# Performance work log

Measured on AMD Instinct MI355X. Metric: run time of the kernel, lower is better.

## Reference

```python
import jax, jax.numpy as jnp
import numpy as np

B, S, E, H = 2, 2048, 1024, 16
HD = E // H


def setup_inputs() -> dict:
    key = jax.random.key(0)
    ks = jax.random.split(key, 5)
    scale = 0.02
    return {
        "x": jax.random.normal(ks[0], (B, S, E), dtype=jnp.float32),
        "qkv_w": jax.random.normal(ks[1], (3 * E, E), dtype=jnp.float32) * scale,
        "qkv_b": jax.random.normal(ks[2], (3 * E,), dtype=jnp.float32) * scale,
        "out_w": jax.random.normal(ks[3], (E, E), dtype=jnp.float32) * scale,
        "out_b": jax.random.normal(ks[4], (E,), dtype=jnp.float32) * scale,
    }


def reference(x, qkv_w, qkv_b, out_w, out_b):
    b, s, e = x.shape
    scale = 1.0 / jnp.sqrt(jnp.float32(HD))
    # fused QKV projection: torch Linear is x @ W.T + b
    qkv = x @ qkv_w.T + qkv_b                       # [b, s, 3e]
    qkv = qkv.reshape(b, s, 3, H, HD)
    qkv = jnp.transpose(qkv, (2, 0, 3, 1, 4))       # [3, b, h, s, hd]
    q, k, v = qkv[0], qkv[1], qkv[2]
    scores = jnp.einsum('bhqd,bhkd->bhqk', q, k) * scale
    # causal mask (atmask=True): mask strictly upper triangle
    causal = jnp.triu(jnp.ones((s, s), dtype=bool), k=1)
    scores = jnp.where(causal, -jnp.inf, scores)
    attn = jax.nn.softmax(scores, axis=-1)          # dropout p=0.0 -> identity
    out = jnp.einsum('bhqk,bhkd->bhqd', attn, v)    # [b, h, s, hd]
    out = jnp.transpose(out, (0, 2, 1, 3)).reshape(b, s, e)
    return out @ out_w.T + out_b
```

## Files before the change

kernel.cpp:

```cpp
#include <hip/hip_runtime.h>
#include <cmath>

typedef __attribute__((ext_vector_type(8))) __bf16 bf16x8;
typedef __attribute__((ext_vector_type(8))) unsigned short ushort8v;
typedef __attribute__((ext_vector_type(4))) float f32x4;

__device__ inline unsigned short f2bf(float f) {
    unsigned int u = __float_as_uint(f);
    unsigned int r = (u + 0x7fffu + ((u >> 16) & 1u)) >> 16;
    return (unsigned short)r;
}

__device__ inline bf16x8 ld8(const unsigned short* p) {
    uint4 v = *(const uint4*)p;
    return __builtin_bit_cast(bf16x8, v);
}

__device__ inline f32x4 mfma16(bf16x8 a, bf16x8 b, f32x4 c) {
    return __builtin_amdgcn_mfma_f32_16x16x32_bf16(a, b, c, 0, 0, 0);
}

__device__ inline unsigned pk2t(float a, float b) {
    return __builtin_amdgcn_perm(__float_as_uint(b), __float_as_uint(a), 0x07060302u);
}

__device__ inline void gl_lds16(const unsigned short* g, const unsigned short* l) {
    __builtin_amdgcn_global_load_lds(
        (const __attribute__((address_space(1))) void*)(unsigned long long)g,
        (__attribute__((address_space(3))) void*)(unsigned)(unsigned long long)l,
        16, 0, 0);
}

#define NX4  1048576
#define NW14 786432
#define NW24 262144
__global__ __launch_bounds__(256) void cvt3(const float* __restrict__ x,
                                            const float* __restrict__ w1,
                                            const float* __restrict__ w2,
                                            unsigned short* __restrict__ xb,
                                            unsigned short* __restrict__ w1b,
                                            unsigned short* __restrict__ w2b) {
    int i = blockIdx.x * 256 + threadIdx.x;
    const float* src;
    unsigned short* dst;
    int off;
    if (i < NX4)              { src = x;  dst = xb;  off = i; }
    else if (i < NX4 + NW14)  { src = w1; dst = w1b; off = i - NX4; }
    else                      { src = w2; dst = w2b; off = i - NX4 - NW14; }
    float4 v = ((const float4*)src)[off];
    ushort4 o;
    o.x = f2bf(v.x); o.y = f2bf(v.y); o.z = f2bf(v.z); o.w = f2bf(v.w);
    ((ushort4*)dst)[off] = o;
}

__global__ __launch_bounds__(256) void gemm_out(const unsigned short* __restrict__ A,
                                                const unsigned short* __restrict__ B,
                                                const float* __restrict__ bias,
                                                float* __restrict__ C,
                                                int M, int N, int K) {
    __shared__ __align__(16) unsigned short As0[64 * 32];
    __shared__ __align__(16) unsigned short Bs0[128 * 32];
    __shared__ __align__(16) unsigned short As1[64 * 32];
    __shared__ __align__(16) unsigned short Bs1[128 * 32];
    const int m0 = blockIdx.y * 64;
    const int n0 = blockIdx.x * 128;
    const int t = threadIdx.x;
    const int wave = t >> 6, lane = t & 63;
    const int l16 = lane & 15, quad = lane >> 4;
    const int wm = (wave >> 1) * 32, wn = (wave & 1) * 64;

    f32x4 acc[2][4] = {};

    const int ra = t >> 2, ka = (t & 3) * 8;
    const int b1 = 256 + t;
    const int rb0 = t >> 2, kb0 = (t & 3) * 8;
    const int rb1 = b1 >> 2, kb1 = (b1 & 3) * 8;

    for (int k0 = 0; k0 < K; k0 += 64) {
        __syncthreads();
        gl_lds16(A + (size_t)(m0 + ra) * K + k0 + ka,        As0 + t * 8);
        gl_lds16(B + (size_t)(n0 + rb0) * K + k0 + kb0,      Bs0 + t * 8);
        gl_lds16(B + (size_t)(n0 + rb1) * K + k0 + kb1,      Bs0 + b1 * 8);
        gl_lds16(A + (size_t)(m0 + ra) * K + k0 + 32 + ka,   As1 + t * 8);
        gl_lds16(B + (size_t)(n0 + rb0) * K + k0 + 32 + kb0, Bs1 + t * 8);
        gl_lds16(B + (size_t)(n0 + rb1) * K + k0 + 32 + kb1, Bs1 + b1 * 8);
        __syncthreads();

        bf16x8 af[2], bfr[4];
        #pragma unroll
        for (int i = 0; i < 2; ++i)
            af[i] = ld8(As0 + (wm + i * 16 + l16) * 32 + quad * 8);
        #pragma unroll
        for (int j = 0; j < 4; ++j)
            bfr[j] = ld8(Bs0 + (wn + j * 16 + l16) * 32 + quad * 8);
        #pragma unroll
        for (int i = 0; i < 2; ++i)
            #pragma unroll
            for (int j = 0; j < 4; ++j)
                acc[i][j] = mfma16(af[i], bfr[j], acc[i][j]);

        #pragma unroll
        for (int i = 0; i < 2; ++i)
            af[i] = ld8(As1 + (wm + i * 16 + l16) * 32 + quad * 8);
        #pragma unroll
        for (int j = 0; j < 4; ++j)
            bfr[j] = ld8(Bs1 + (wn + j * 16 + l16) * 32 + quad * 8);
        #pragma unroll
        for (int i = 0; i < 2; ++i)
            #pragma unroll
            for (int j = 0; j < 4; ++j)
                acc[i][j] = mfma16(af[i], bfr[j], acc[i][j]);
    }

    #pragma unroll
    for (int i = 0; i < 2; ++i) {
        #pragma unroll
        for (int j = 0; j < 4; ++j) {
            int col = n0 + wn + j * 16 + l16;
            float bv = bias[col];
            #pragma unroll
            for (int r = 0; r < 4; ++r) {
                int row = m0 + wm + i * 16 + quad * 4 + r;
                C[(size_t)row * N + col] = acc[i][j][r] + bv;
            }
        }
    }
}

__global__ __launch_bounds__(256) void gemm_qkv(const unsigned short* __restrict__ A,
                                                const unsigned short* __restrict__ B,
                                                const float* __restrict__ bias,
                                                unsigned short* __restrict__ qp,
                                                unsigned short* __restrict__ kvp,
                                                int M, int N, int K) {
    __shared__ __align__(16) unsigned short Ep[16384];
    unsigned short* As0 = Ep;
    unsigned short* Bs0 = Ep + 4096;
    unsigned short* As1 = Ep + 8192;
    unsigned short* Bs1 = Ep + 12288;
    const int m0 = blockIdx.y * 128;
    const int n0 = blockIdx.x * 128;
    const int t = threadIdx.x;
    const int wave = t >> 6, lane = t & 63;
    const int l16 = lane & 15, quad = lane >> 4;
    const int wm = (wave >> 1) * 64, wn = (wave & 1) * 64;

    f32x4 acc[4][4] = {};

    const int ra = t >> 2, ka = (t & 3) * 8;

    for (int k0 = 0; k0 < K; k0 += 64) {
        __syncthreads();
        gl_lds16(A + (size_t)(m0 + ra) * K + k0 + ka,           As0 + t * 8);
        gl_lds16(A + (size_t)(m0 + 64 + ra) * K + k0 + ka,      As0 + 2048 + t * 8);
        gl_lds16(B + (size_t)(n0 + ra) * K + k0 + ka,           Bs0 + t * 8);
        gl_lds16(B + (size_t)(n0 + 64 + ra) * K + k0 + ka,      Bs0 + 2048 + t * 8);
        gl_lds16(A + (size_t)(m0 + ra) * K + k0 + 32 + ka,      As1 + t * 8);
        gl_lds16(A + (size_t)(m0 + 64 + ra) * K + k0 + 32 + ka, As1 + 2048 + t * 8);
        gl_lds16(B + (size_t)(n0 + ra) * K + k0 + 32 + ka,      Bs1 + t * 8);
        gl_lds16(B + (size_t)(n0 + 64 + ra) * K + k0 + 32 + ka, Bs1 + 2048 + t * 8);
        __syncthreads();

        bf16x8 af[4], bfr[4];
        #pragma unroll
        for (int i = 0; i < 4; ++i)
            af[i] = ld8(As0 + (wm + i * 16 + l16) * 32 + quad * 8);
        #pragma unroll
        for (int j = 0; j < 4; ++j)
            bfr[j] = ld8(Bs0 + (wn + j * 16 + l16) * 32 + quad * 8);
        #pragma unroll
        for (int i = 0; i < 4; ++i)
            #pragma unroll
            for (int j = 0; j < 4; ++j)
                acc[i][j] = mfma16(af[i], bfr[j], acc[i][j]);

        #pragma unroll
        for (int i = 0; i < 4; ++i)
            af[i] = ld8(As1 + (wm + i * 16 + l16) * 32 + quad * 8);
        #pragma unroll
        for (int j = 0; j < 4; ++j)
            bfr[j] = ld8(Bs1 + (wn + j * 16 + l16) * 32 + quad * 8);
        #pragma unroll
        for (int i = 0; i < 4; ++i)
            #pragma unroll
            for (int j = 0; j < 4; ++j)
                acc[i][j] = mfma16(af[i], bfr[j], acc[i][j]);
    }

    __syncthreads();
    const int b = m0 >> 11;

    if (n0 < 1024) {
        #pragma unroll
        for (int j = 0; j < 4; ++j) {
            int cl = wn + j * 16 + l16;
            float bv = bias[n0 + cl];
            int hrel = cl >> 6, d = cl & 63;
            int half = d >> 5, qd = d & 31;
            int obase = hrel * 8192 + half * 512 + (qd >> 3) * 128 + quad * 32 + (qd & 7);
            #pragma unroll
            for (int i = 0; i < 4; ++i) {
                int ob = obase + ((wm + i * 16) >> 4) * 1024;
                #pragma unroll
                for (int r = 0; r < 4; ++r)
                    Ep[ob + r * 8] = f2bf((acc[i][j][r] + bv) * 0.180336880f);
            }
        }
        __syncthreads();
        const int h0 = n0 >> 6, qt0 = (m0 & 2047) >> 4;
        #pragma unroll
        for (int k = 0; k < 8; ++k) {
            int u = t + 256 * k;
            int cq = u >> 7, within = u & 127;
            int bh = b * 16 + h0 + (cq >> 3);
            int qt = qt0 + (cq & 7);
            *(uint4*)(qp + (size_t)(bh * 128 + qt) * 1024 + within * 8) =
                *(const uint4*)(Ep + u * 8);
        }
    } else if (n0 < 2048) {
        const int f2 = (quad & 1) * 2, qh = 4 * (quad >> 1);
        #pragma unroll
        for (int j = 0; j < 4; ++j) {
            int cl = wn + j * 16 + l16;
            float bv = bias[n0 + cl];
            int hrel = cl >> 6, d = cl & 63;
            int fbit0 = d >> 5, qd = d & 31;
            int obase = hrel * 8192 + (f2 | fbit0) * 512 +
                        (qd >> 3) * 128 + qh * 8 + (qd & 7);
            #pragma unroll
            for (int i = 0; i < 4; ++i) {
                int ob = obase + ((wm >> 5) + (i >> 1)) * 2048 + (i & 1) * 64;
                #pragma unroll
                for (int r = 0; r < 4; ++r)
                    Ep[ob + r * 8] = f2bf(acc[i][j][r] + bv);
            }
        }
        __syncthreads();
        const int h0 = (n0 - 1024) >> 6, tile0 = (m0 & 2047) >> 5;
        #pragma unroll
        for (int k = 0; k < 8; ++k) {
            int u = t + 256 * k;
            int ck = u >> 8, within = u & 255;
            int bh = b * 16 + h0 + (ck >> 2);
            int tile = tile0 + (ck & 3);
            *(uint4*)(kvp + (size_t)(bh * 64 + tile) * 4096 + within * 8) =
                *(const uint4*)(Ep + u * 8);
        }
    } else {
        const int kr = quad >> 1, e4 = (quad & 1) * 4;
        #pragma unroll
        for (int j = 0; j < 4; ++j) {
            int cl = wn + j * 16 + l16;
            float bv = bias[n0 + cl];
            int hrel = cl >> 6, d = cl & 63;
            int tn = d >> 4, l16v = d & 15;
            int obase = hrel * 8192 + tn * 512 + (kr * 16 + l16v) * 8 + e4;
            #pragma unroll
            for (int i = 0; i < 4; ++i) {
                int ob = obase + ((wm >> 5) + (i >> 1)) * 2048 + (i & 1) * 256;
                unsigned short tmp[4];
                #pragma unroll
                for (int r = 0; r < 4; ++r) tmp[r] = f2bf(acc[i][j][r] + bv);
                *(unsigned long long*)(Ep + ob) = *(const unsigned long long*)tmp;
            }
        }
        __syncthreads();
        const int h0 = (n0 - 2048) >> 6, tile0 = (m0 & 2047) >> 5;
        #pragma unroll
        for (int k = 0; k < 8; ++k) {
            int u = t + 256 * k;
            int ck = u >> 8, within = u & 255;
            int bh = b * 16 + h0 + (ck >> 2);
            int tile = tile0 + (ck & 3);
            *(uint4*)(kvp + (size_t)(bh * 64 + tile) * 4096 + 2048 + within * 8) =
                *(const uint4*)(Ep + u * 8);
        }
    }
}

__global__ __launch_bounds__(256, 2) void attn_kernel(const unsigned short* __restrict__ qp,
                                                      const unsigned short* __restrict__ kvp,
                                                      unsigned short* __restrict__ out) {
    const int S = 2048, E = 1024;
    const int wavei = threadIdx.x >> 6;
    const int lane = threadIdx.x & 63;
    const int l16 = lane & 15, quad = lane >> 4;
    const int bidx = blockIdx.x;
    const int bh = (bidx & 7) * 4 + ((bidx >> 3) & 3);
    const int P = 31 - (bidx >> 5);
    const int b = bh >> 4, h = bh & 15;
    const int loff = lane * 8;

    const unsigned short* qbase = qp + (size_t)(bh * 128 + 4 * P) * 1024;
    bf16x8 bq[4][2];
    #pragma unroll
    for (int g = 0; g < 4; ++g) {
        bq[g][0] = ld8(qbase + (2 * g) * 512 + loff);
        bq[g][1] = ld8(qbase + (2 * g + 1) * 512 + loff);
    }

    ushort8v ov;
    #pragma unroll
    for (int j = 0; j < 8; ++j) ov[j] = 0x3F80;
    const bf16x8 ones = __builtin_bit_cast(bf16x8, ov);

    f32x4 O[4][4] = {};
    f32x4 L[4] = {};
    const int nchunks = P + 1;
    const unsigned short* tbase = kvp + (size_t)bh * 64 * 4096;

    for (int c = wavei; c < nchunks; c += 4) {
        const unsigned short* tb = tbase + (size_t)c * 8192;
        bf16x8 f[16];
        #pragma unroll
        for (int i = 0; i < 16; ++i) f[i] = ld8(tb + i * 512 + loff);

        const bool lastc = (c == nchunks - 1);
        const int ks = c * 64;

        #pragma unroll
        for (int tile = 0; tile < 2; ++tile) {
            const bf16x8* g8 = f + tile * 8;
            const int kst = ks + tile * 32;

            f32x4 s0[4], s1[4];
            #pragma unroll
            for (int g = 0; g < 4; ++g) { s0[g] = {}; s1[g] = {}; }
            #pragma unroll
            for (int g = 0; g < 4; ++g) {
                s0[g] = mfma16(g8[0], bq[g][0], s0[g]);
                s0[g] = mfma16(g8[1], bq[g][1], s0[g]);
                s1[g] = mfma16(g8[2], bq[g][0], s1[g]);
                s1[g] = mfma16(g8[3], bq[g][1], s1[g]);
            }

            bf16x8 bp[4];
            #pragma unroll
            for (int g = 0; g < 4; ++g) {
                float p0[4], p1[4];
                if (lastc) {
                    const int qg = 64 * P + 16 * g + l16;
                    #pragma unroll
                    for (int r = 0; r < 4; ++r) {
                        int kk = kst + quad * 8 + r;
                        p0[r] = (kk > qg)     ? 0.f : __builtin_amdgcn_exp2f(s0[g][r]);
                        p1[r] = (kk + 4 > qg) ? 0.f : __builtin_amdgcn_exp2f(s1[g][r]);
                    }
                } else {
                    #pragma unroll
                    for (int r = 0; r < 4; ++r) {
                        p0[r] = __builtin_amdgcn_exp2f(s0[g][r]);
                        p1[r] = __builtin_amdgcn_exp2f(s1[g][r]);
                    }
                }
                uint4 pw;
                pw.x = pk2t(p0[0], p0[1]);
                pw.y = pk2t(p0[2], p0[3]);
                pw.z = pk2t(p1[0], p1[1]);
                pw.w = pk2t(p1[2], p1[3]);
                bp[g] = __builtin_bit_cast(bf16x8, pw);
            }

            #pragma unroll
            for (int g = 0; g < 4; ++g) {
                O[g][0] = mfma16(g8[4], bp[g], O[g][0]);
                O[g][1] = mfma16(g8[5], bp[g], O[g][1]);
                O[g][2] = mfma16(g8[6], bp[g], O[g][2]);
                O[g][3] = mfma16(g8[7], bp[g], O[g][3]);
                L[g]    = mfma16(ones, bp[g], L[g]);
            }
        }
    }

    __shared__ float Ob[4][64][66];
    __shared__ float Lb[4][64];
    #pragma unroll
    for (int g = 0; g < 4; ++g) {
        #pragma unroll
        for (int tn = 0; tn < 4; ++tn)
            #pragma unroll
            for (int r = 0; r < 4; ++r)
                Ob[wavei][g * 16 + l16][tn * 16 + quad * 4 + r] = O[g][tn][r];
        if (quad == 0) Lb[wavei][g * 16 + l16] = L[g][0];
    }
    __syncthreads();

    const int t = threadIdx.x;
    const int qi = t >> 2, hg = (t & 3) * 16;
    float ls = Lb[0][qi] + Lb[1][qi] + Lb[2][qi] + Lb[3][qi];
    const float invl = 1.0f / ls;
    const size_t obase = (size_t)(b * S + 64 * P + qi) * E + h * 64;
    #pragma unroll
    for (int part = 0; part < 2; ++part) {
        int hd0 = hg + part * 8;
        unsigned short o[8];
        #pragma unroll
        for (int k = 0; k < 8; ++k) {
            float a = Ob[0][qi][hd0 + k] + Ob[1][qi][hd0 + k] +
                      Ob[2][qi][hd0 + k] + Ob[3][qi][hd0 + k];
            o[k] = f2bf(a * invl);
        }
        *(uint4*)(out + obase + hd0) = *(uint4*)o;
    }
}

extern "C" void kernel_launch(void* const* d_in, const int* in_sizes, int n_in,
                              void* d_out, int out_size, void* d_ws, size_t ws_size,
                              hipStream_t stream) {
    const float* x     = (const float*)d_in[0];
    const float* qkv_w = (const float*)d_in[1];
    const float* qkv_b = (const float*)d_in[2];
    const float* out_w = (const float*)d_in[3];
    const float* out_b = (const float*)d_in[4];
    float* out = (float*)d_out;

    const int B = 2, S = 2048, E = 1024;
    const int M = B * S;
    const int N1 = 3 * E;

    unsigned short* ws    = (unsigned short*)d_ws;
    unsigned short* xb    = ws;
    unsigned short* w1b   = xb   + (size_t)M * E;
    unsigned short* w2b   = w1b  + (size_t)N1 * E;
    unsigned short* qpb   = w2b  + (size_t)E * E;
    unsigned short* kvpb  = qpb  + (size_t)32 * 128 * 1024;
    unsigned short* attnb = kvpb + (size_t)32 * 64 * 4096;

    cvt3<<<dim3(8192), dim3(256), 0, stream>>>(x, qkv_w, out_w, xb, w1b, w2b);

    gemm_qkv<<<dim3(N1 / 128, M / 128), dim3(256), 0, stream>>>(
        xb, w1b, qkv_b, qpb, kvpb, M, N1, E);

    attn_kernel<<<dim3(1024), dim3(256), 0, stream>>>(qpb, kvpb, attnb);

    gemm_out<<<dim3(E / 128, M / 64), dim3(256), 0, stream>>>(
        attnb, w2b, out_b, out, M, E, E);
}
```

Baseline: 170.1 us.

## Rewrite QKV GEMM as 256x256 tile with pipelined swizzled LDS staging

The QKV projection GEMM moves from 128x128 tiles with 256 threads to 256x256 tiles with 512 threads and a 128KB LDS buffer. Global-to-LDS loads are double-buffered and interleaved with MFMA phases, using explicit vmcnt waits, barriers and setprio. An XOR swizzle on the LDS layout is meant to avoid bank conflicts. The epilogue is reorganised into four chunked passes through LDS. The aim is more operand reuse and overlap of loads with compute, at the cost of only 48 blocks (occupancy 1) and hardcoded K=1024 and iteration counts.

```diff
diff --git a/kernel.cpp b/kernel.cpp
--- a/kernel.cpp
+++ b/kernel.cpp
@@ -127,155 +127,227 @@
     }
 }
 
-__global__ __launch_bounds__(256) void gemm_qkv(const unsigned short* __restrict__ A,
-                                                const unsigned short* __restrict__ B,
-                                                const float* __restrict__ bias,
-                                                unsigned short* __restrict__ qp,
-                                                unsigned short* __restrict__ kvp,
-                                                int M, int N, int K) {
-    __shared__ __align__(16) unsigned short Ep[16384];
-    unsigned short* As0 = Ep;
-    unsigned short* Bs0 = Ep + 4096;
-    unsigned short* As1 = Ep + 8192;
-    unsigned short* Bs1 = Ep + 12288;
-    const int m0 = blockIdx.y * 128;
-    const int n0 = blockIdx.x * 128;
+__global__ __launch_bounds__(512, 1) void gemm_qkv(const unsigned short* __restrict__ A,
+                                                   const unsigned short* __restrict__ B,
+                                                   const float* __restrict__ bias,
+                                                   unsigned short* __restrict__ qp,
+                                                   unsigned short* __restrict__ kvp,
+                                                   int M, int N, int K) {
+    __shared__ __align__(16) unsigned short L_[65536];
+    const int m0 = blockIdx.y * 256;
+    const int n0 = blockIdx.x * 256;
     const int t = threadIdx.x;
     const int wave = t >> 6, lane = t & 63;
     const int l16 = lane & 15, quad = lane >> 4;
-    const int wm = (wave >> 1) * 64, wn = (wave & 1) * 64;
-
-    f32x4 acc[4][4] = {};
-
-    const int ra = t >> 2, ka = (t & 3) * 8;
-
-    for (int k0 = 0; k0 < K; k0 += 64) {
-        __syncthreads();
-        gl_lds16(A + (size_t)(m0 + ra) * K + k0 + ka,           As0 + t * 8);
-        gl_lds16(A + (size_t)(m0 + 64 + ra) * K + k0 + ka,      As0 + 2048 + t * 8);
-        gl_lds16(B + (size_t)(n0 + ra) * K + k0 + ka,           Bs0 + t * 8);
-        gl_lds16(B + (size_t)(n0 + 64 + ra) * K + k0 + ka,      Bs0 + 2048 + t * 8);
-        gl_lds16(A + (size_t)(m0 + ra) * K + k0 + 32 + ka,      As1 + t * 8);
-        gl_lds16(A + (size_t)(m0 + 64 + ra) * K + k0 + 32 + ka, As1 + 2048 + t * 8);
-        gl_lds16(B + (size_t)(n0 + ra) * K + k0 + 32 + ka,      Bs1 + t * 8);
-        gl_lds16(B + (size_t)(n0 + 64 + ra) * K + k0 + 32 + ka, Bs1 + 2048 + t * 8);
-        __syncthreads();
-
-        bf16x8 af[4], bfr[4];
-        #pragma unroll
-        for (int i = 0; i < 4; ++i)
-            af[i] = ld8(As0 + (wm + i * 16 + l16) * 32 + quad * 8);
-        #pragma unroll
-        for (int j = 0; j < 4; ++j)
-            bfr[j] = ld8(Bs0 + (wn + j * 16 + l16) * 32 + quad * 8);
-        #pragma unroll
-        for (int i = 0; i < 4; ++i)
-            #pragma unroll
-            for (int j = 0; j < 4; ++j)
-                acc[i][j] = mfma16(af[i], bfr[j], acc[i][j]);
-
-        #pragma unroll
-        for (int i = 0; i < 4; ++i)
-            af[i] = ld8(As1 + (wm + i * 16 + l16) * 32 + quad * 8);
-        #pragma unroll
-        for (int j = 0; j < 4; ++j)
-            bfr[j] = ld8(Bs1 + (wn + j * 16 + l16) * 32 + quad * 8);
-        #pragma unroll
-        for (int i = 0; i < 4; ++i)
-            #pragma unroll
-            for (int j = 0; j < 4; ++j)
-                acc[i][j] = mfma16(af[i], bfr[j], acc[i][j]);
-    }
+    const int wr = wave >> 2, wc = wave & 3;
+    const int rswz = (l16 & 7) << 3;
+
+    f32x4 acc[8][4] = {};
+    bf16x8 bf[4][2];
+
+    const int c0 = t, c1 = 512 + t;
+    const int r0 = c0 >> 3, k0e = ((c0 & 7) ^ (r0 & 7)) * 8;
+    const int r1 = c1 >> 3, k1e = ((c1 & 7) ^ (r1 & 7)) * 8;
+    const unsigned short* Ab0 = A + (size_t)(m0 + r0) * 1024 + k0e;
+    const unsigned short* Ab1 = A + (size_t)(m0 + r1) * 1024 + k1e;
+    const unsigned short* Bb0 = B + (size_t)(n0 + r0) * 1024 + k0e;
+    const unsigned short* Bb1 = B + (size_t)(n0 + r1) * 1024 + k1e;
+    unsigned short* Ld0 = L_ + c0 * 8;
+    unsigned short* Ld1 = L_ + c1 * 8;
+
+#define STG_A(par, h, T_) do { \
+    gl_lds16(Ab0 + (h) * 131072 + (T_) * 64, Ld0 + (par) * 16384 + (h) * 8192); \
+    gl_lds16(Ab1 + (h) * 131072 + (T_) * 64, Ld1 + (par) * 16384 + (h) * 8192); } while (0)
+#define STG_B(par, h, T_) do { \
+    gl_lds16(Bb0 + (h) * 131072 + (T_) * 64, Ld0 + 32768 + (par) * 16384 + (h) * 8192); \
+    gl_lds16(Bb1 + (h) * 131072 + (T_) * 64, Ld1 + 32768 + (par) * 16384 + (h) * 8192); } while (0)
+
+    const unsigned short* Afr = L_ + wr * 8192 + l16 * 64;
+    const unsigned short* Bfr = L_ + 32768 + (wc >> 1) * 8192 + ((wc & 1) * 64 + l16) * 64;
+    const int koff0 = (quad * 8) ^ rswz;
+    const int koff1 = (32 + quad * 8) ^ rswz;
+
+#define LDA0(dst, par, i_) dst = ld8(Afr + (par) * 16384 + (i_) * 1024 + koff0)
+#define LDA1(dst, par, i_) dst = ld8(Afr + (par) * 16384 + (i_) * 1024 + koff1)
+#define LDB0(dst, par, j_) dst = ld8(Bfr + (par) * 16384 + (j_) * 1024 + koff0)
+#define LDB1(dst, par, j_) dst = ld8(Bfr + (par) * 16384 + (j_) * 1024 + koff1)
+
+#define FEN() asm volatile("" ::: "memory")
+#define BARR() do { FEN(); __builtin_amdgcn_s_barrier(); FEN(); } while (0)
+#define VM4 asm volatile("s_waitcnt vmcnt(4)" ::: "memory")
+#define VM0 asm volatile("s_waitcnt vmcnt(0)" ::: "memory")
+#define VMN ((void)0)
+
+#define PHASE(PAR, I0, LOADB, STG, VM) do { \
+    bf16x8 a00, a01, a10, a11; \
+    if (LOADB) { \
+        LDB0(bf[0][0], PAR, 0); LDB1(bf[0][1], PAR, 0); \
+        LDB0(bf[1][0], PAR, 1); LDB1(bf[1][1], PAR, 1); \
+        LDB0(bf[2][0], PAR, 2); LDB1(bf[2][1], PAR, 2); \
+        LDB0(bf[3][0], PAR, 3); LDB1(bf[3][1], PAR, 3); \
+    } \
+    LDA0(a00, PAR, I0); LDA1(a01, PAR, I0); \
+    LDA0(a10, PAR, (I0) + 1); LDA1(a11, PAR, (I0) + 1); \
+    STG; \
+    BARR(); \
+    __builtin_amdgcn_s_setprio(1); \
+    acc[I0][0] = mfma16(a00, bf[0][0], acc[I0][0]); \
+    acc[I0][1] = mfma16(a00, bf[1][0], acc[I0][1]); \
+    acc[I0][2] = mfma16(a00, bf[2][0], acc[I0][2]); \
+    acc[I0][3] = mfma16(a00, bf[3][0], acc[I0][3]); \
+    acc[(I0)+1][0] = mfma16(a10, bf[0][0], acc[(I0)+1][0]); \
+    acc[(I0)+1][1] = mfma16(a10, bf[1][0], acc[(I0)+1][1]); \
+    acc[(I0)+1][2] = mfma16(a10, bf[2][0], acc[(I0)+1][2]); \
+    acc[(I0)+1][3] = mfma16(a10, bf[3][0], acc[(I0)+1][3]); \
+    acc[I0][0] = mfma16(a01, bf[0][1], acc[I0][0]); \
+    acc[I0][1] = mfma16(a01, bf[1][1], acc[I0][1]); \
+    acc[I0][2] = mfma16(a01, bf[2][1], acc[I0][2]); \
+    acc[I0][3] = mfma16(a01, bf[3][1], acc[I0][3]); \
+    acc[(I0)+1][0] = mfma16(a11, bf[0][1], acc[(I0)+1][0]); \
+    acc[(I0)+1][1] = mfma16(a11, bf[1][1], acc[(I0)+1][1]); \
+    acc[(I0)+1][2] = mfma16(a11, bf[2][1], acc[(I0)+1][2]); \
+    acc[(I0)+1][3] = mfma16(a11, bf[3][1], acc[(I0)+1][3]); \
+    __builtin_amdgcn_s_setprio(0); \
+    VM; \
+    BARR(); \
+} while (0)
+
+    STG_A(0, 0, 0); STG_A(0, 1, 0); STG_B(0, 0, 0); STG_B(0, 1, 0);
+    STG_B(1, 0, 1); STG_B(1, 1, 1);
+    VM4;
+    BARR();
+
+    for (int it = 0; it < 7; ++it) {
+        const int T = 2 * it;
+        PHASE(0, 0, 1, STG_A(1, 0, T + 1), VMN);
+        PHASE(0, 2, 0, STG_A(1, 1, T + 1), VMN);
+        PHASE(0, 4, 0, STG_B(0, 0, T + 2), VMN);
+        PHASE(0, 6, 0, STG_B(0, 1, T + 2), VM4);
+        PHASE(1, 0, 1, STG_A(0, 0, T + 2), VMN);
+        PHASE(1, 2, 0, STG_A(0, 1, T + 2), VMN);
+        PHASE(1, 4, 0, STG_B(1, 0, T + 3), VMN);
+        PHASE(1, 6, 0, STG_B(1, 1, T + 3), VM4);
+    }
+    PHASE(0, 0, 1, STG_A(1, 0, 15), VMN);
+    PHASE(0, 2, 0, STG_A(1, 1, 15), VMN);
+    PHASE(0, 4, 0, VMN, VMN);
+    PHASE(0, 6, 0, VMN, VM0);
+    PHASE(1, 0, 1, VMN, VMN);
+    PHASE(1, 2, 0, VMN, VMN);
+    PHASE(1, 4, 0, VMN, VMN);
+    PHASE(1, 6, 0, VMN, VMN);
 
     __syncthreads();
     const int b = m0 >> 11;
 
     if (n0 < 1024) {
-        #pragma unroll
-        for (int j = 0; j < 4; ++j) {
-            int cl = wn + j * 16 + l16;
-            float bv = bias[n0 + cl];
-            int hrel = cl >> 6, d = cl & 63;
-            int half = d >> 5, qd = d & 31;
-            int obase = hrel * 8192 + half * 512 + (qd >> 3) * 128 + quad * 32 + (qd & 7);
-            #pragma unroll
-            for (int i = 0; i < 4; ++i) {
-                int ob = obase + ((wm + i * 16) >> 4) * 1024;
+        const int h0 = n0 >> 6, qt0 = (m0 & 2047) >> 4;
+        #pragma unroll
+        for (int c = 0; c < 4; ++c) {
+            #pragma unroll
+            for (int j = 0; j < 4; ++j) {
+                float bv = bias[n0 + wc * 64 + j * 16 + l16];
+                int half = j >> 1, qd = (j & 1) * 16 + l16;
+                int obase = (wc * 4 + wr * 2) * 1024 + half * 512 +
+                            (qd >> 3) * 128 + quad * 32 + (qd & 7);
                 #pragma unroll
-                for (int r = 0; r < 4; ++r)
-                    Ep[ob + r * 8] = f2bf((acc[i][j][r] + bv) * 0.180336880f);
-            }
-        }
-        __syncthreads();
-        const int h0 = n0 >> 6, qt0 = (m0 & 2047) >> 4;
-        #pragma unroll
-        for (int k = 0; k < 8; ++k) {
-            int u = t + 256 * k;
-            int cq = u >> 7, within = u & 127;
-            int bh = b * 16 + h0 + (cq >> 3);
-            int qt = qt0 + (cq & 7);
-            *(uint4*)(qp + (size_t)(bh * 128 + qt) * 1024 + within * 8) =
-                *(const uint4*)(Ep + u * 8);
+                for (int li = 0; li < 2; ++li) {
+                    int ob = obase + li * 1024;
+                    #pragma unroll
+                    for (int r = 0; r < 4; ++r)
+                        L_[ob + r * 8] = f2bf((acc[2 * c + li][j][r] + bv) * 0.180336880f);
+                }
+            }
+            __syncthreads();
+            #pragma unroll
+            for (int kk = 0; kk < 4; ++kk) {
+                int u = t + 512 * kk;
+                int unit = u >> 7, within = u & 127;
+                int wcp = unit >> 2, slot = unit & 3;
+                int qt = qt0 + (slot >> 1) * 8 + c * 2 + (slot & 1);
+                int bh = b * 16 + h0 + wcp;
+                *(uint4*)(qp + (size_t)(bh * 128 + qt) * 1024 + within * 8) =
+                    *(const uint4*)(L_ + u * 8);
+            }
+            __syncthreads();
         }
     } else if (n0 < 2048) {
+        const int h0 = (n0 - 1024) >> 6, tile0 = (m0 & 2047) >> 5;
         const int f2 = (quad & 1) * 2, qh = 4 * (quad >> 1);
         #pragma unroll
-        for (int j = 0; j < 4; ++j) {
-            int cl = wn + j * 16 + l16;
-            float bv = bias[n0 + cl];
-            int hrel = cl >> 6, d = cl & 63;
-            int fbit0 = d >> 5, qd = d & 31;
-            int obase = hrel * 8192 + (f2 | fbit0) * 512 +
-                        (qd >> 3) * 128 + qh * 8 + (qd & 7);
-            #pragma unroll
-            for (int i = 0; i < 4; ++i) {
-                int ob = obase + ((wm >> 5) + (i >> 1)) * 2048 + (i & 1) * 64;
+        for (int c = 0; c < 4; ++c) {
+            #pragma unroll
+            for (int j = 0; j < 4; ++j) {
+                float bv = bias[n0 + wc * 64 + j * 16 + l16];
+                int d = j * 16 + l16;
+                int fbit0 = d >> 5, qd = d & 31;
+                int obase = (wc * 2 + wr) * 2048 + (f2 | fbit0) * 512 +
+                            (qd >> 3) * 128 + qh * 8 + (qd & 7);
                 #pragma unroll
-                for (int r = 0; r < 4; ++r)
-                    Ep[ob + r * 8] = f2bf(acc[i][j][r] + bv);
-            }
-        }
-        __syncthreads();
-        const int h0 = (n0 - 1024) >> 6, tile0 = (m0 & 2047) >> 5;
-        #pragma unroll
-        for (int k = 0; k < 8; ++k) {
-            int u = t + 256 * k;
-            int ck = u >> 8, within = u & 255;
-            int bh = b * 16 + h0 + (ck >> 2);
-            int tile = tile0 + (ck & 3);
-            *(uint4*)(kvp + (size_t)(bh * 64 + tile) * 4096 + within * 8) =
-                *(const uint4*)(Ep + u * 8);
+                for (int li = 0; li < 2; ++li) {
+                    int ob = obase + li * 64;
+                    #pragma unroll
+                    for (int r = 0; r < 4; ++r)
+                        L_[ob + r * 8] = f2bf(acc[2 * c + li][j][r] + bv);
+                }
+            }
+            __syncthreads();
+            #pragma unroll
+            for (int kk = 0; kk < 4; ++kk) {
+                int u = t + 512 * kk;
+                int unit = u >> 8, within = u & 255;
+                int wcp = unit >> 1, wrp = unit & 1;
+                int bh = b * 16 + h0 + wcp;
+                int tile = tile0 + wrp * 4 + c;
+                *(uint4*)(kvp + (size_t)(bh * 64 + tile) * 4096 + within * 8) =
+                    *(const uint4*)(L_ + u * 8);
+            }
+            __syncthreads();
         }
     } else {
+        const int h0 = (n0 - 2048) >> 6, tile0 = (m0 & 2047) >> 5;
         const int kr = quad >> 1, e4 = (quad & 1) * 4;
         #pragma unroll
-        for (int j = 0; j < 4; ++j) {
-            int cl = wn + j * 16 + l16;
-            float bv = bias[n0 + cl];
-            int hrel = cl >> 6, d = cl & 63;
-            int tn = d >> 4, l16v = d & 15;
-            int obase = hrel * 8192 + tn * 512 + (kr * 16 + l16v) * 8 + e4;
-            #pragma unroll
-            for (int i = 0; i < 4; ++i) {
-                int ob = obase + ((wm >> 5) + (i >> 1)) * 2048 + (i & 1) * 256;
-                unsigned short tmp[4];
+        for (int c = 0; c < 4; ++c) {
+            #pragma unroll
+            for (int j = 0; j < 4; ++j) {
+                float bv = bias[n0 + wc * 64 + j * 16 + l16];
+                int obase = (wc * 2 + wr) * 2048 + j * 512 + (kr * 16 + l16) * 8 + e4;
                 #pragma unroll
-                for (int r = 0; r < 4; ++r) tmp[r] = f2bf(acc[i][j][r] + bv);
-                *(unsigned long long*)(Ep + ob) = *(const unsigned long long*)tmp;
-            }
+                for (int li = 0; li < 2; ++li) {
+                    int ob = obase + li * 256;
+                    unsigned short tmp[4];
+                    #pragma unroll
+                    for (int r = 0; r < 4; ++r) tmp[r] = f2bf(acc[2 * c + li][j][r] + bv);
+                    *(unsigned long long*)(L_ + ob) = *(const unsigned long long*)tmp;
+                }
+            }
+            __syncthreads();
+            #pragma unroll
+            for (int kk = 0; kk < 4; ++kk) {
+                int u = t + 512 * kk;
+                int unit = u >> 8, within = u & 255;
+                int wcp = unit >> 1, wrp = unit & 1;
+                int bh = b * 16 + h0 + wcp;
+                int tile = tile0 + wrp * 4 + c;
+                *(uint4*)(kvp + (size_t)(bh * 64 + tile) * 4096 + 2048 + within * 8) =
+                    *(const uint4*)(L_ + u * 8);
+            }
+            __syncthreads();
         }
-        __syncthreads();
-        const int h0 = (n0 - 2048) >> 6, tile0 = (m0 & 2047) >> 5;
-        #pragma unroll
-        for (int k = 0; k < 8; ++k) {
-            int u = t + 256 * k;
-            int ck = u >> 8, within = u & 255;
-            int bh = b * 16 + h0 + (ck >> 2);
-            int tile = tile0 + (ck & 3);
-            *(uint4*)(kvp + (size_t)(bh * 64 + tile) * 4096 + 2048 + within * 8) =
-                *(const uint4*)(Ep + u * 8);
-        }
-    }
+    }
+#undef STG_A
+#undef STG_B
+#undef LDA0
+#undef LDA1
+#undef LDB0
+#undef LDB1
+#undef FEN
+#undef BARR
+#undef VM4
+#undef VM0
+#undef VMN
+#undef PHASE
 }
 
 __global__ __launch_bounds__(256, 2) void attn_kernel(const unsigned short* __restrict__ qp,
@@ -428,7 +500,7 @@
 
     cvt3<<<dim3(8192), dim3(256), 0, stream>>>(x, qkv_w, out_w, xb, w1b, w2b);
 
-    gemm_qkv<<<dim3(N1 / 128, M / 128), dim3(256), 0, stream>>>(
+    gemm_qkv<<<dim3(N1 / 256, M / 256), dim3(512), 0, stream>>>(
         xb, w1b, qkv_b, qpb, kvpb, M, N1, E);
 
     attn_kernel<<<dim3(1024), dim3(256), 0, stream>>>(qpb, kvpb, attnb);
```

After: 162.8 us. -4.3%, faster.
